# Kernel optimization log

Measured on AMD Instinct MI355X. Metric: run time of the kernel, lower is better.

Reference implementation:

```python
import jax, jax.numpy as jnp
import numpy as np

T, D, DFF, E, K, CAP = 8192, 1024, 4096, 8, 2, 2560


def setup_inputs() -> dict:
    key = jax.random.key(0)
    ks = jax.random.split(key, 6)
    return {
        "x_flat": jax.random.normal(ks[0], (T, D), dtype=jnp.float32),
        "idx_flat": jax.random.randint(ks[1], (T, K), 0, E, dtype=jnp.int32),
        "scores_flat": jax.random.uniform(ks[2], (T, K), dtype=jnp.float32),
        "capacity": CAP,
        "W1": jax.random.normal(ks[3], (E, D, DFF), dtype=jnp.float32) * 0.02,
        "B1": jnp.zeros((E, DFF), dtype=jnp.float32),
        "W2": jax.random.normal(ks[4], (E, DFF, D), dtype=jnp.float32) * 0.02,
        "B2": jnp.zeros((E, D), dtype=jnp.float32),
    }


def reference(x_flat, idx_flat, scores_flat, capacity, W1, B1, W2, B2):
    # Fused MoE dispatch: capacity-limited gather -> per-expert FFN (grouped GEMM)
    # -> weighted scatter-combine.
    Ttok, d = x_flat.shape
    k = idx_flat.shape[1]
    e = idx_flat.reshape(-1)                      # [T*k] expert id per assignment
    s = scores_flat.reshape(-1)                   # [T*k] gate score
    tok = jnp.repeat(jnp.arange(Ttok), k)         # [T*k] source token index

    oh = jax.nn.one_hot(e, W1.shape[0], dtype=jnp.int32)   # [T*k, E]
    # slot of each assignment within its expert (0-based arrival order)
    pos = jnp.sum(jnp.cumsum(oh, axis=0) * oh, axis=1) - 1  # [T*k]
    keep = pos < capacity                                   # drop overflow tokens
    pos_c = jnp.where(keep, pos, 0)

    # gather tokens into per-expert buffers [E, capacity, d]
    xe = jnp.zeros((W1.shape[0], capacity, d), dtype=x_flat.dtype)
    xe = xe.at[e, pos_c].add(jnp.where(keep[:, None], x_flat[tok], 0.0))

    # per-expert FFN (grouped GEMM)
    h = jax.nn.gelu(jnp.einsum('ecd,edf->ecf', xe, W1) + B1[:, None, :])
    y = jnp.einsum('ecf,efd->ecd', h, W2) + B2[:, None, :]   # [E, capacity, d]

    # scatter back, scaled by gate scores
    yg = y[e, pos_c] * (s * keep.astype(s.dtype))[:, None]   # [T*k, d]
    out = jnp.zeros_like(x_flat).at[tok].add(yg)
    return out
```

## Files before the change

### kernel.cpp

```cpp
#include <hip/hip_runtime.h>
#include <hip/hip_bf16.h>

#define T_TOK   8192
#define D_MODEL 1024
#define DFF     4096
#define N_EXP   8
#define TOPK    2
#define CAP     2560
#define NASSIGN (T_TOK * TOPK)

typedef unsigned short u16;
typedef __attribute__((ext_vector_type(8))) short  short8;
typedef __attribute__((ext_vector_type(8))) unsigned short u16x8;
typedef __attribute__((ext_vector_type(4))) float  f32x4;


__device__ inline u16 f2bf(float f) {
    union { float f; unsigned u; } v; v.f = f;
    unsigned u = v.u;
    unsigned r = (u + 0x7fffu + ((u >> 16) & 1u)) >> 16;
    return (u16)r;
}

__device__ inline float gelu_tanh(float x) {
    float z = 0.7978845608028654f * (x + 0.044715f * x * x * x);
    z = fminf(fmaxf(z, -15.f), 15.f);
    float ez = __expf(2.f * z);
    float t = (ez - 1.f) / (ez + 1.f);
    return 0.5f * x * (1.f + t);
}

__device__ inline void gload_lds16(const void* g, void* l) {
    __builtin_amdgcn_global_load_lds(
        (const __attribute__((address_space(1))) unsigned int*)g,
        (__attribute__((address_space(3))) unsigned int*)l, 16, 0, 0);
}

__device__ __forceinline__ void BARm() {
    asm volatile("" ::: "memory");
    __builtin_amdgcn_sched_barrier(0);
    __builtin_amdgcn_s_barrier();
    __builtin_amdgcn_sched_barrier(0);
    asm volatile("" ::: "memory");
}

__global__ __launch_bounds__(256) void scan_kernel(
    const int* __restrict__ idx, int* __restrict__ counts,
    int* __restrict__ pos_arr, int* __restrict__ slot_src)
{
    const int eb = blockIdx.x;
    const int tid = threadIdx.x;
    __shared__ int sbuf[256];
    const int CHUNK = NASSIGN / 256;
    const int base_i = tid * CHUNK;
    int local = 0;
    #pragma unroll 8
    for (int j = 0; j < CHUNK; ++j) local += (idx[base_i + j] == eb) ? 1 : 0;
    sbuf[tid] = local;
    __syncthreads();
    for (int off = 1; off < 256; off <<= 1) {
        int v = (tid >= off) ? sbuf[tid - off] : 0;
        __syncthreads();
        sbuf[tid] += v;
        __syncthreads();
    }
    int run = sbuf[tid] - local;
    for (int j = 0; j < CHUNK; ++j) {
        int i = base_i + j;
        if (idx[i] == eb) {
            if (run < CAP) { pos_arr[i] = run; slot_src[eb * CAP + run] = i / TOPK; }
            else           { pos_arr[i] = -1; }
            ++run;
        }
    }
    if (tid == 0) {
        int tot = sbuf[255];
        counts[eb] = tot < CAP ? tot : CAP;
    }
}

__global__ __launch_bounds__(256) void transpose_cvt(
    const float* __restrict__ in, u16* __restrict__ out, int R, int C)
{
    __shared__ float tile[32][33];
    const int e = blockIdx.z;
    const int c0 = blockIdx.x * 32, r0 = blockIdx.y * 32;
    const float* ine = in + (size_t)e * R * C;
    u16* oute = out + (size_t)e * R * C;
    const int tx = threadIdx.x, ty = threadIdx.y;
    #pragma unroll
    for (int i = 0; i < 4; ++i) {
        int r = ty + i * 8;
        tile[r][tx] = ine[(size_t)(r0 + r) * C + c0 + tx];
    }
    __syncthreads();
    #pragma unroll
    for (int i = 0; i < 4; ++i) {
        int cr = ty + i * 8;
        oute[(size_t)(c0 + cr) * R + r0 + tx] = f2bf(tile[tx][cr]);
    }
}

__global__ __launch_bounds__(128) void gather_kernel(
    const float* __restrict__ x, const int* __restrict__ counts,
    const int* __restrict__ slot_src, u16* __restrict__ Xe)
{
    const int b = blockIdx.x;
    const int e = b / CAP, slot = b % CAP;
    const int tid = threadIdx.x;
    u16* dst = Xe + ((size_t)e * CAP + slot) * D_MODEL + tid * 8;
    if (slot < counts[e]) {
        const int tok = slot_src[b];
        const float4* src = (const float4*)(x + (size_t)tok * D_MODEL) + tid * 2;
        float4 a = src[0], c = src[1];
        u16x8 v;
        v[0] = f2bf(a.x); v[1] = f2bf(a.y); v[2] = f2bf(a.z); v[3] = f2bf(a.w);
        v[4] = f2bf(c.x); v[5] = f2bf(c.y); v[6] = f2bf(c.z); v[7] = f2bf(c.w);
        *(u16x8*)dst = v;
    } else {
        float4 z = {0.f, 0.f, 0.f, 0.f};
        *(float4*)dst = z;
    }
}

template<int KD, int ND, bool FUSE_GELU>
__global__ __launch_bounds__(512, 2) void gemm8(
    const u16* __restrict__ A, const u16* __restrict__ Bt,
    const float* __restrict__ bias, void* __restrict__ Cout,
    const int* __restrict__ counts, int nx, int ny)
{
    __shared__ __align__(16) char lds[131072];

    const int nwg = nx * ny * N_EXP;
    const int cpx = nwg >> 3;
    const int id2 = (blockIdx.x & 7) * cpx + (blockIdx.x >> 3);
    const int e   = id2 / (nx * ny);
    const int rem = id2 % (nx * ny);
    const int bx = rem % nx, by = rem / nx;
    const int brow = bx << 8;
    if (brow >= counts[e]) return;
    const int bcol = by << 8;

    const int tid = threadIdx.x;
    const char* Ae = (const char*)(A + ((size_t)e * CAP + brow) * KD);
    const char* Be = (const char*)(Bt + ((size_t)e * ND + bcol) * KD);
    constexpr int RB = KD * 2;
    constexpr int NT = KD / 64;

    const int lane = tid & 63;
    const int wid = tid >> 6;
    const int wm = wid >> 2, wn = wid & 3;
    const int lr = lane & 15, lq = lane >> 4;

    const int srow0 = tid >> 2, ss = tid & 3;

    #define STG(gbase, buf, slot, kb) do {                                         \
        { int row_ = srow0;       int sl_ = ss ^ ((row_ >> 1) & 3);                \
          gload_lds16((gbase) + (size_t)row_ * RB + (kb) + sl_ * 16,               \
                      lds + (buf) * 65536 + (slot) * 16384 + tid * 16); }          \
        { int row_ = 128 + srow0; int sl_ = ss ^ ((row_ >> 1) & 3);                \
          gload_lds16((gbase) + (size_t)row_ * RB + (kb) + sl_ * 16,               \
                      lds + (buf) * 65536 + (slot) * 16384 + 8192 + tid * 16); }   \
    } while (0)

    auto RD = [&](int buf, int slot, int row) -> short8 {
        int sl = lq ^ ((row >> 1) & 3);
        return *(const short8*)(lds + buf * 65536 + slot * 16384 + row * 64 + sl * 16);
    };

    f32x4 acc[8][4] = {};
    short8 af[4], bf[4];

    #define MFMA16(MB) do {                                                        \
        __builtin_amdgcn_s_setprio(1);                                             \
        _Pragma("unroll")                                                          \
        for (int m_ = 0; m_ < 4; ++m_)                                             \
            _Pragma("unroll")                                                      \
            for (int n_ = 0; n_ < 4; ++n_)                                         \
                acc[(MB) + m_][n_] = __builtin_amdgcn_mfma_f32_16x16x32_bf16(      \
                    af[m_], bf[n_], acc[(MB) + m_][n_], 0, 0, 0);                  \
        __builtin_amdgcn_s_setprio(0);                                             \
    } while (0)

    STG(Ae, 0, 0, 0);
    STG(Be, 0, 2, 0);
    STG(Ae, 0, 1, 64);
    STG(Be, 0, 3, 64);
    STG(Ae, 1, 0, 128);
    STG(Be, 1, 2, 128);
    asm volatile("s_waitcnt vmcnt(4)" ::: "memory");
    BARm();

    for (int t = 0; t < NT; ++t) {
        const int buf = t & 1;
        const int obuf = buf ^ 1;

        #pragma unroll
        for (int n = 0; n < 4; ++n) bf[n] = RD(buf, 2, wn * 64 + n * 16 + lr);
        #pragma unroll
        for (int m = 0; m < 4; ++m) af[m] = RD(buf, 0, wm * 128 + m * 16 + lr);
        if (t + 1 < NT) STG(Ae, obuf, 1, (t + 1) * 128 + 64);
        BARm();
        MFMA16(0);
        BARm();

        #pragma unroll
        for (int m = 0; m < 4; ++m) af[m] = RD(buf, 0, wm * 128 + (4 + m) * 16 + lr);
        if (t + 1 < NT) STG(Be, obuf, 3, (t + 1) * 128 + 64);
        BARm();
        MFMA16(4);
        BARm();

        #pragma unroll
        for (int n = 0; n < 4; ++n) bf[n] = RD(buf, 3, wn * 64 + n * 16 + lr);
        #pragma unroll
        for (int m = 0; m < 4; ++m) af[m] = RD(buf, 1, wm * 128 + m * 16 + lr);
        if (t + 2 < NT) STG(Ae, buf, 0, (t + 2) * 128);
        BARm();
        MFMA16(0);
        BARm();

        #pragma unroll
        for (int m = 0; m < 4; ++m) af[m] = RD(buf, 1, wm * 128 + (4 + m) * 16 + lr);
        if (t + 2 < NT) STG(Be, buf, 2, (t + 2) * 128);
        BARm();
        MFMA16(4);
        if (t + 2 < NT)      { asm volatile("s_waitcnt vmcnt(4)" ::: "memory"); }
        else if (t + 1 < NT) { asm volatile("s_waitcnt vmcnt(0)" ::: "memory"); }
        BARm();
    }

    const float* be = bias + (size_t)e * ND + bcol;
    if (FUSE_GELU) {
        u16* Ce = (u16*)Cout + ((size_t)e * CAP + brow) * ND + bcol;
        #pragma unroll
        for (int m = 0; m < 8; ++m)
            #pragma unroll
            for (int n = 0; n < 4; ++n) {
                f32x4 v = acc[m][n];
                int c = wn * 64 + n * 16 + lr;
                float bb = be[c];
                #pragma unroll
                for (int j = 0; j < 4; ++j) {
                    int r = wm * 128 + m * 16 + lq * 4 + j;
                    Ce[(size_t)r * ND + c] = f2bf(gelu_tanh(v[j] + bb));
                }
            }
    } else {
        float* Ce = (float*)Cout + ((size_t)e * CAP + brow) * ND + bcol;
        #pragma unroll
        for (int m = 0; m < 8; ++m)
            #pragma unroll
            for (int n = 0; n < 4; ++n) {
                f32x4 v = acc[m][n];
                int c = wn * 64 + n * 16 + lr;
                float bb = be[c];
                #pragma unroll
                for (int j = 0; j < 4; ++j) {
                    int r = wm * 128 + m * 16 + lq * 4 + j;
                    Ce[(size_t)r * ND + c] = v[j] + bb;
                }
            }
    }
    #undef STG
    #undef MFMA16
}

__global__ __launch_bounds__(256) void scatter_kernel(
    const int* __restrict__ idx, const float* __restrict__ scores,
    const int* __restrict__ pos_arr, const float* __restrict__ Y,
    float* __restrict__ out)
{
    const int t = blockIdx.x;
    const int tid = threadIdx.x;
    float4 acc = {0.f, 0.f, 0.f, 0.f};
    #pragma unroll
    for (int k = 0; k < TOPK; ++k) {
        int i = t * TOPK + k;
        int p = pos_arr[i];
        if (p >= 0) {
            int e = idx[i];
            float s = scores[i];
            float4 v = *(const float4*)(Y + ((size_t)e * CAP + p) * D_MODEL + tid * 4);
            acc.x += s * v.x; acc.y += s * v.y; acc.z += s * v.z; acc.w += s * v.w;
        }
    }
    *(float4*)(out + (size_t)t * D_MODEL + tid * 4) = acc;
}

extern "C" void kernel_launch(void* const* d_in, const int* in_sizes, int n_in,
                              void* d_out, int out_size, void* d_ws, size_t ws_size,
                              hipStream_t stream)
{
    const float* x      = (const float*)d_in[0];
    const int*   idx    = (const int*)d_in[1];
    const float* scores = (const float*)d_in[2];
    const float* W1 = (const float*)d_in[4];
    const float* B1 = (const float*)d_in[5];
    const float* W2 = (const float*)d_in[6];
    const float* B2 = (const float*)d_in[7];
    float* out = (float*)d_out;

    char* ws = (char*)d_ws;
    size_t off = 0;
    auto alloc = [&](size_t bytes) {
        char* p = ws + off;
        off += (bytes + 255) & ~(size_t)255;
        return p;
    };
    int* counts   = (int*)alloc(N_EXP * 4);
    int* pos_arr  = (int*)alloc((size_t)NASSIGN * 4);
    int* slot_src = (int*)alloc((size_t)N_EXP * CAP * 4);
    u16* W1b = (u16*)alloc((size_t)N_EXP * D_MODEL * DFF * 2);
    u16* Xe  = (u16*)alloc((size_t)N_EXP * CAP * D_MODEL * 2);
    u16* W2b = (u16*)alloc((size_t)N_EXP * DFF * D_MODEL * 2);
    u16* H   = (u16*)alloc((size_t)N_EXP * CAP * DFF * 2);
    float* Y = (float*)W1b;

    scan_kernel<<<N_EXP, 256, 0, stream>>>(idx, counts, pos_arr, slot_src);
    transpose_cvt<<<dim3(DFF / 32, D_MODEL / 32, N_EXP), dim3(32, 8), 0, stream>>>(
        W1, W1b, D_MODEL, DFF);
    transpose_cvt<<<dim3(D_MODEL / 32, DFF / 32, N_EXP), dim3(32, 8), 0, stream>>>(
        W2, W2b, DFF, D_MODEL);
    gather_kernel<<<N_EXP * CAP, 128, 0, stream>>>(x, counts, slot_src, Xe);
    gemm8<D_MODEL, DFF, true><<<(CAP / 256) * (DFF / 256) * N_EXP, 512, 0, stream>>>(
        Xe, W1b, B1, H, counts, CAP / 256, DFF / 256);
    gemm8<DFF, D_MODEL, false><<<(CAP / 256) * (D_MODEL / 256) * N_EXP, 512, 0, stream>>>(
        H, W2b, B2, Y, counts, CAP / 256, D_MODEL / 256);
    scatter_kernel<<<T_TOK, 256, 0, stream>>>(idx, scores, pos_arr, Y, out);
}
```

Before: 795.7 us.

## Vectorize weight transpose-convert and relax GEMM barrier scheduling fences

The fp32-to-bf16 weight transpose now uses 64x64 tiles, with float4 global loads and 16-byte packed bf16 stores, so fewer, wider memory transactions replace per-element ones. In the grouped GEMM, the sched_barrier-wrapped barriers are replaced by plain s_barrier. Only the tile-boundary fences keep a vmcnt wait plus a memory clobber, which lets the compiler interleave LDS reads and MFMAs more freely. The risk is that the compiler reorders LDS reads across barriers without the memory clobber, and the larger transpose tile raises LDS use.

```diff
diff --git a/kernel.cpp b/kernel.cpp
--- a/kernel.cpp
+++ b/kernel.cpp
@@ -34,14 +34,6 @@
     __builtin_amdgcn_global_load_lds(
         (const __attribute__((address_space(1))) unsigned int*)g,
         (__attribute__((address_space(3))) unsigned int*)l, 16, 0, 0);
-}
-
-__device__ __forceinline__ void BARm() {
-    asm volatile("" ::: "memory");
-    __builtin_amdgcn_sched_barrier(0);
-    __builtin_amdgcn_s_barrier();
-    __builtin_amdgcn_sched_barrier(0);
-    asm volatile("" ::: "memory");
 }
 
 __global__ __launch_bounds__(256) void scan_kernel(
@@ -82,22 +74,29 @@
 __global__ __launch_bounds__(256) void transpose_cvt(
     const float* __restrict__ in, u16* __restrict__ out, int R, int C)
 {
-    __shared__ float tile[32][33];
+    __shared__ float tile[64][65];
     const int e = blockIdx.z;
-    const int c0 = blockIdx.x * 32, r0 = blockIdx.y * 32;
-    const float* ine = in + (size_t)e * R * C;
-    u16* oute = out + (size_t)e * R * C;
-    const int tx = threadIdx.x, ty = threadIdx.y;
+    const int c0 = blockIdx.x * 64, r0 = blockIdx.y * 64;
+    const float* ine = in + (size_t)e * R * C + (size_t)r0 * C + c0;
+    const int tid = threadIdx.x;
     #pragma unroll
     for (int i = 0; i < 4; ++i) {
-        int r = ty + i * 8;
-        tile[r][tx] = ine[(size_t)(r0 + r) * C + c0 + tx];
+        int f = tid + i * 256;
+        int r = f >> 4, c4 = (f & 15) << 2;
+        float4 v = *(const float4*)(ine + (size_t)r * C + c4);
+        tile[r][c4] = v.x; tile[r][c4 + 1] = v.y;
+        tile[r][c4 + 2] = v.z; tile[r][c4 + 3] = v.w;
     }
     __syncthreads();
+    u16* oute = out + (size_t)e * C * R + (size_t)c0 * R + r0;
     #pragma unroll
-    for (int i = 0; i < 4; ++i) {
-        int cr = ty + i * 8;
-        oute[(size_t)(c0 + cr) * R + r0 + tx] = f2bf(tile[tx][cr]);
+    for (int i = 0; i < 2; ++i) {
+        int o = tid + i * 256;
+        int c = o >> 3, r8 = (o & 7) << 3;
+        u16x8 v;
+        #pragma unroll
+        for (int j = 0; j < 8; ++j) v[j] = f2bf(tile[r8 + j][c]);
+        *(u16x8*)(oute + (size_t)c * R + r8) = v;
     }
 }
 
@@ -182,14 +181,20 @@
         __builtin_amdgcn_s_setprio(0);                                             \
     } while (0)
 
+    #define BAR() __builtin_amdgcn_s_barrier()
+    #define TILE_FENCE(N) do {                                                     \
+        asm volatile("s_waitcnt vmcnt(" #N ")" ::: "memory");                      \
+        __builtin_amdgcn_s_barrier();                                              \
+        asm volatile("" ::: "memory");                                             \
+    } while (0)
+
     STG(Ae, 0, 0, 0);
     STG(Be, 0, 2, 0);
     STG(Ae, 0, 1, 64);
     STG(Be, 0, 3, 64);
     STG(Ae, 1, 0, 128);
     STG(Be, 1, 2, 128);
-    asm volatile("s_waitcnt vmcnt(4)" ::: "memory");
-    BARm();
+    TILE_FENCE(4);
 
     for (int t = 0; t < NT; ++t) {
         const int buf = t & 1;
@@ -200,34 +205,34 @@
         #pragma unroll
         for (int m = 0; m < 4; ++m) af[m] = RD(buf, 0, wm * 128 + m * 16 + lr);
         if (t + 1 < NT) STG(Ae, obuf, 1, (t + 1) * 128 + 64);
-        BARm();
+        BAR();
         MFMA16(0);
-        BARm();
+        BAR();
 
         #pragma unroll
         for (int m = 0; m < 4; ++m) af[m] = RD(buf, 0, wm * 128 + (4 + m) * 16 + lr);
         if (t + 1 < NT) STG(Be, obuf, 3, (t + 1) * 128 + 64);
-        BARm();
+        BAR();
         MFMA16(4);
-        BARm();
+        BAR();
 
         #pragma unroll
         for (int n = 0; n < 4; ++n) bf[n] = RD(buf, 3, wn * 64 + n * 16 + lr);
         #pragma unroll
         for (int m = 0; m < 4; ++m) af[m] = RD(buf, 1, wm * 128 + m * 16 + lr);
         if (t + 2 < NT) STG(Ae, buf, 0, (t + 2) * 128);
-        BARm();
+        BAR();
         MFMA16(0);
-        BARm();
+        BAR();
 
         #pragma unroll
         for (int m = 0; m < 4; ++m) af[m] = RD(buf, 1, wm * 128 + (4 + m) * 16 + lr);
         if (t + 2 < NT) STG(Be, buf, 2, (t + 2) * 128);
-        BARm();
+        BAR();
         MFMA16(4);
-        if (t + 2 < NT)      { asm volatile("s_waitcnt vmcnt(4)" ::: "memory"); }
-        else if (t + 1 < NT) { asm volatile("s_waitcnt vmcnt(0)" ::: "memory"); }
-        BARm();
+        if (t + 2 < NT)      { TILE_FENCE(4); }
+        else if (t + 1 < NT) { TILE_FENCE(0); }
+        else                 { BAR(); }
     }
 
     const float* be = bias + (size_t)e * ND + bcol;
@@ -264,6 +269,8 @@
     }
     #undef STG
     #undef MFMA16
+    #undef BAR
+    #undef TILE_FENCE
 }
 
 __global__ __launch_bounds__(256) void scatter_kernel(
@@ -318,9 +325,9 @@
     float* Y = (float*)W1b;
 
     scan_kernel<<<N_EXP, 256, 0, stream>>>(idx, counts, pos_arr, slot_src);
-    transpose_cvt<<<dim3(DFF / 32, D_MODEL / 32, N_EXP), dim3(32, 8), 0, stream>>>(
+    transpose_cvt<<<dim3(DFF / 64, D_MODEL / 64, N_EXP), 256, 0, stream>>>(
         W1, W1b, D_MODEL, DFF);
-    transpose_cvt<<<dim3(D_MODEL / 32, DFF / 32, N_EXP), dim3(32, 8), 0, stream>>>(
+    transpose_cvt<<<dim3(D_MODEL / 64, DFF / 64, N_EXP), 256, 0, stream>>>(
         W2, W2b, DFF, D_MODEL);
     gather_kernel<<<N_EXP * CAP, 128, 0, stream>>>(x, counts, slot_src, Xe);
     gemm8<D_MODEL, DFF, true><<<(CAP / 256) * (DFF / 256) * N_EXP, 512, 0, stream>>>(
```

Result: no change. 797.7 us (+0.2%).
